# Kernel tuning notes

Hardware: AMD Instinct MI355X
Metric: run time of the kernel (lower is better)

Reference implementation:

```python
import jax, jax.numpy as jnp
import numpy as np

L = 3
NC = (L + 1) ** 2                                   # 16 spherical components l=0..3
SO3_SIZES = [(2 * l + 1) ** 2 for l in range(L + 1)]  # [1,9,25,49]
SO3_OFF = np.cumsum([0] + SO3_SIZES).tolist()         # [0,1,10,35,84]
D3 = SO3_OFF[-1]                                      # 84 = dim of SO(3) signal irreps
MUL_SIZES = [2 * l + 1 for l in range(L + 1)]         # [1,3,5,7]
MUL_OFF = np.cumsum([0] + MUL_SIZES).tolist()         # [0,1,4,9,16]
LIDX = jnp.array(sum([[l] * (2 * l + 1) for l in range(L + 1)], []))  # comp -> l map (16,)
B, NPG = 32, 256
N = B * NPG
E = 32768
F = 16
MAXR = 3.5
NG = 4096


def real_sh(v):
    # component-normalized real spherical harmonics l=0..3 for unit vectors v (...,3)
    x, y, z = v[..., 0], v[..., 1], v[..., 2]
    s3, s5, s15 = 3.0 ** 0.5, 5.0 ** 0.5, 15.0 ** 0.5
    c = [jnp.ones_like(x),
         s3 * y, s3 * z, s3 * x,
         s15 * x * y, s15 * y * z, 0.5 * s5 * (3 * z * z - 1.0), s15 * x * z, 0.5 * s15 * (x * x - y * y),
         (35.0 / 8.0) ** 0.5 * y * (3 * x * x - y * y),
         105.0 ** 0.5 * x * y * z,
         (21.0 / 8.0) ** 0.5 * y * (5 * z * z - 1.0),
         0.5 * 7.0 ** 0.5 * (5 * z ** 3 - 3 * z),
         (21.0 / 8.0) ** 0.5 * x * (5 * z * z - 1.0),
         0.5 * 105.0 ** 0.5 * (x * x - y * y) * z,
         (35.0 / 8.0) ** 0.5 * x * (x * x - 3 * y * y)]
    return jnp.stack(c, axis=-1)


def gate(h):
    # equivariant gate: relu on l=0 scalars, sigmoid(scalar)-gated l>0 components
    s = h[..., 0:1]
    return jnp.concatenate([jax.nn.relu(s), h[..., 1:] * jax.nn.sigmoid(s)], axis=-1)


def setup_inputs() -> dict:
    key = jax.random.key(0)
    ks = jax.random.split(key, 16)
    rn = lambda k, s, sc=1.0: jax.random.normal(k, s, dtype=jnp.float32) * sc
    return {
        'node_feat': rn(ks[0], (N, F)),
        'pos': rn(ks[1], (N, 3), 1.5),
        'orientation': jax.random.uniform(ks[2], (B, 2), dtype=jnp.float32) * jnp.pi,
        'rad1_W1': rn(ks[3], (1, 64)),
        'rad1_b': jnp.zeros((64,), jnp.float32),
        'rad1_W2': rn(ks[4], (64, 2048), 0.1),
        'rad2_W1': rn(ks[5], (1, 64)),
        'rad2_b': jnp.zeros((64,), jnp.float32),
        'rad2_W2': rn(ks[6], (64, 2176), 0.1),
        'Wlin': rn(ks[7], (2 * F, F, NC)),
        'psi1': rn(ks[8], (16, 64, D3)),
        'psi2': rn(ks[9], (64, 128, D3)),
        'psi3': rn(ks[10], (128, 256, D3)),
        'G_to': rn(ks[11], (D3, NG)),
        'G_from': rn(ks[12], (NG, D3)),
        'Ws2': rn(ks[13], (256, 1, NC)),
        'edge_src': jax.random.randint(ks[14], (E,), 0, N, dtype=jnp.int32),
        'edge_dst': jax.random.randint(ks[15], (E,), 0, N, dtype=jnp.int32),
        'batch': jnp.repeat(jnp.arange(B, dtype=jnp.int32), NPG),
    }


def reference(node_feat, pos, orientation, rad1_W1, rad1_b, rad1_W2, rad2_W1, rad2_b,
              rad2_W2, Wlin, psi1, psi2, psi3, G_to, G_from, Ws2,
              edge_src, edge_dst, batch):
    # ---- encoder: radius-graph equivariant message passing (gather / TP / scatter) ----
    ev = pos[edge_dst] - pos[edge_src]
    d = jnp.linalg.norm(ev, axis=-1) + 1e-9
    Y = real_sh(ev / d[:, None])                              # (E,16) edge SH
    u = d / MAXR
    cut = jnp.where(u < 1.0, 0.5 * (jnp.cos(jnp.pi * u) + 1.0), 0.0)

    def radial(W1, b, W2):
        hh = jax.nn.relu(u[:, None] * W1 + b)                 # (E,64)
        return (hh @ W2) * cut[:, None]

    deg = (E / N) ** 0.5
    # layer 1: scalar-in x SH tensor product with per-edge radial weights
    w1 = radial(rad1_W1, rad1_b, rad1_W2).reshape(E, F, F, 2, L + 1)
    t1 = jnp.einsum('ef,efgpl->egpl', node_feat[edge_src], w1) / (F ** 0.5)
    msg1 = t1[:, :, :, LIDX] * Y[:, None, None, :]            # (E,16,2,16)
    h1 = jax.ops.segment_sum(msg1, edge_dst, num_segments=N) / deg
    h1 = gate(h1)
    # layer 2: scalar x SH path + l_in (x) 0e self path
    w2 = radial(rad2_W1, rad2_b, rad2_W2)
    w2sh = w2[:, :2048].reshape(E, F, F, 2, L + 1)
    w2self = w2[:, 2048:].reshape(E, F, 2, L + 1)
    t2 = jnp.einsum('ef,efgpl->egpl', h1[:, :, 0, 0][edge_src], w2sh) / (F ** 0.5)
    msg2 = t2[:, :, :, LIDX] * Y[:, None, None, :] + h1[edge_src] * w2self[:, :, :, LIDX]
    h2 = jax.ops.segment_sum(msg2, edge_dst, num_segments=N) / deg
    h2 = gate(h2)
    # mean-pool readout per graph -> (B, 512)
    cnt = jax.ops.segment_sum(jnp.ones((N,), h2.dtype), batch, num_segments=B)
    enc = jax.ops.segment_sum(h2.reshape(N, -1), batch, num_segments=B) / cnt[:, None]

    # ---- o3.Linear enc_out -> so3_irreps latent z (B, F, 84) ----
    e = enc.reshape(B, 2 * F, NC)
    zs = []
    for l in range(L + 1):
        c0, c1 = MUL_OFF[l], MUL_OFF[l + 1]
        zl = jnp.einsum('bmc,mgj->bgjc', e[:, :, c0:c1], Wlin[:, :, c0:c1]) / (2 * F) ** 0.5
        zs.append(zl.reshape(B, F, -1))
    z = jnp.concatenate(zs, axis=-1)

    # ---- decoder: SO(3) equivariant convs + grid activations ----
    def so3_conv(x, psi):
        fi, fo = psi.shape[0], psi.shape[1]
        outs = []
        for l in range(L + 1):
            o0, o1 = SO3_OFF[l], SO3_OFF[l + 1]
            m = 2 * l + 1
            xl = x[:, :, o0:o1].reshape(B, fi, m, m)
            pl = psi[:, :, o0:o1].reshape(fi, fo, m, m)
            ol = jnp.einsum('bfic,fgij->bgjc', xl, pl) / (fi * m) ** 0.5
            outs.append(ol.reshape(B, fo, m * m))
        return jnp.concatenate(outs, axis=-1)

    def so3_act(x):
        g = jax.nn.relu(jnp.einsum('bfd,dg->bfg', x, G_to) / D3 ** 0.5)
        return jnp.einsum('bfg,gd->bfd', g, G_from) / NG ** 0.5

    x = so3_act(so3_conv(z, psi1))
    x = so3_act(so3_conv(x, psi2))
    x = so3_act(so3_conv(x, psi3))

    # ---- SO3 -> S2 convolution -> (B, out_dim, 16) ----
    outs = []
    for l in range(L + 1):
        o0, o1 = SO3_OFF[l], SO3_OFF[l + 1]
        m = 2 * l + 1
        xl = x[:, :, o0:o1].reshape(B, 256, m, m)
        Wl = Ws2[:, :, MUL_OFF[l]:MUL_OFF[l + 1]]
        outs.append(jnp.einsum('bfic,fgi->bgc', xl, Wl) / (256 * m) ** 0.5)
    s2 = jnp.concatenate(outs, axis=-1)

    # ---- aspect/roll -> cartesian line-of-sight -> SH response (bmm) ----
    a, r = orientation[..., 0], orientation[..., 1]
    cart = jnp.stack([-jnp.sin(a) * jnp.cos(r), -jnp.sin(a) * jnp.sin(r), -jnp.cos(a)], axis=-1)
    shp = real_sh(cart)                                       # (B,16)
    return jnp.einsum('bgc,bc->bg', s2, shp)[:, 0]            # (B,)
```

## Files before the change

kernel.cpp:

```cpp
#include <hip/hip_runtime.h>
#include <math.h>

#define DEV static __device__ __forceinline__

constexpr int NN = 8192;
constexpr int NE = 32768;
constexpr int NB = 32;

using short8 = __attribute__((ext_vector_type(8))) short;
using f32x4  = __attribute__((ext_vector_type(4))) float;

DEV ushort f2bf(float f) {
  unsigned u = __float_as_uint(f);
  unsigned r = (u + 0x7FFFu + ((u >> 16) & 1u)) >> 16;
  return (ushort)r;
}
DEV float bf2f(ushort h) { return __uint_as_float(((unsigned)h) << 16); }

DEV void split8(const float* p, short8& hi, short8& lo) {
#pragma unroll
  for (int j = 0; j < 8; ++j) {
    const ushort h = f2bf(p[j]);
    hi[j] = (short)h;
    const float r = p[j] - bf2f(h);
    lo[j] = (short)(__float_as_uint(r) >> 16);
  }
}

DEV int lidx_of(int c) { return (c == 0) ? 0 : (c < 4) ? 1 : (c < 9) ? 2 : 3; }

DEV void real_sh_f(float x, float y, float z, float* Y) {
  const float s3  = 1.7320508075688772f;
  const float s5  = 2.23606797749979f;
  const float s15 = 3.872983346207417f;
  Y[0] = 1.f;
  Y[1] = s3 * y;  Y[2] = s3 * z;  Y[3] = s3 * x;
  Y[4] = s15 * x * y;
  Y[5] = s15 * y * z;
  Y[6] = 0.5f * s5 * (3.f * z * z - 1.f);
  Y[7] = s15 * x * z;
  Y[8] = 0.5f * s15 * (x * x - y * y);
  Y[9]  = 2.091650066335189f * y * (3.f * x * x - y * y);
  Y[10] = 10.246950765959598f * x * y * z;
  Y[11] = 1.6201851746019651f * y * (5.f * z * z - 1.f);
  Y[12] = 1.3228756555322954f * (5.f * z * z * z - 3.f * z);
  Y[13] = 1.6201851746019651f * x * (5.f * z * z - 1.f);
  Y[14] = 5.123475382979799f * (x * x - y * y) * z;
  Y[15] = 2.091650066335189f * x * (x * x - 3.f * y * y);
}

__global__ __launch_bounds__(256) void k_edge_prep(
    const float* __restrict__ pos, const int* __restrict__ esrc,
    const int* __restrict__ edst, float* __restrict__ u_, float* __restrict__ cut_,
    float* __restrict__ Y_, int* __restrict__ cnt) {
  const int e = blockIdx.x * 256 + threadIdx.x;
  if (e >= NE) return;
  const int s = esrc[e], t = edst[e];
  const float ex = pos[t * 3 + 0] - pos[s * 3 + 0];
  const float ey = pos[t * 3 + 1] - pos[s * 3 + 1];
  const float ez = pos[t * 3 + 2] - pos[s * 3 + 2];
  const float d = sqrtf(ex * ex + ey * ey + ez * ez) + 1e-9f;
  const float inv = 1.f / d;
  float Y[16];
  real_sh_f(ex * inv, ey * inv, ez * inv, Y);
#pragma unroll
  for (int c = 0; c < 16; ++c) Y_[(size_t)e * 16 + c] = Y[c];
  const float u = d / 3.5f;
  u_[e] = u;
  cut_[e] = (u < 1.f) ? 0.5f * (cosf(3.14159265358979323846f * u) + 1.f) : 0.f;
  atomicAdd(&cnt[t], 1);
}

__global__ __launch_bounds__(256) void k_scan(const int* __restrict__ cnt,
                                              int* __restrict__ offs,
                                              int* __restrict__ cursor) {
  __shared__ int part[256];
  const int t = threadIdx.x;
  int s = 0;
  for (int i = 0; i < 32; ++i) s += cnt[t * 32 + i];
  part[t] = s;
  __syncthreads();
  if (t == 0) {
    int run = 0;
    for (int i = 0; i < 256; ++i) { int v = part[i]; part[i] = run; run += v; }
    offs[NN] = run;
  }
  __syncthreads();
  int run = part[t];
  for (int i = 0; i < 32; ++i) {
    const int idx = t * 32 + i;
    offs[idx] = run;
    cursor[idx] = run;
    run += cnt[idx];
  }
}

__global__ __launch_bounds__(256) void k_fill(const int* __restrict__ edst,
                                              int* __restrict__ cursor,
                                              int* __restrict__ elist) {
  const int e = blockIdx.x * 256 + threadIdx.x;
  if (e < NE) {
    const int p = atomicAdd(&cursor[edst[e]], 1);
    elist[p] = e;
  }
}

template <bool IS2>
__global__ __launch_bounds__(256) void k_prep_w2t(const float* __restrict__ W2,
                                                  ushort* __restrict__ Th,
                                                  ushort* __restrict__ Tl) {
  const int idx = blockIdx.x * 256 + threadIdx.x;
  if (idx >= 128 * 1024) return;
  const int o = idx >> 10, kf = idx & 1023;
  const float v = IS2 ? W2[(size_t)(kf >> 4) * 2176 + (kf & 15) * 128 + o]
                      : W2[(size_t)kf * 128 + o];
  const ushort h = f2bf(v);
  Th[idx] = h;
  Tl[idx] = (ushort)(__float_as_uint(v - bf2f(h)) >> 16);
}

__global__ __launch_bounds__(256) void k_prep_selfw(const float* __restrict__ W2,
                                                    ushort* __restrict__ Sh,
                                                    ushort* __restrict__ Sl) {
  const int idx = blockIdx.x * 256 + threadIdx.x;
  if (idx >= 128 * 64) return;
  const int o = idx >> 6, k = idx & 63;
  const float v = W2[(size_t)k * 2176 + 2048 + o];
  const ushort h = f2bf(v);
  Sh[idx] = h;
  Sl[idx] = (ushort)(__float_as_uint(v - bf2f(h)) >> 16);
}

#define MSG_STEP(HS, BH, BL)                                                     \
  do {                                                                           \
    short8 ah_[2], al_[2];                                                       \
    _Pragma("unroll") for (int mt = 0; mt < 2; ++mt) {                           \
      float p_[8];                                                               \
      _Pragma("unroll") for (int j = 0; j < 8; ++j) p_[j] = HS[mt] * nf8[mt][j]; \
      split8(p_, ah_[mt], al_[mt]);                                              \
    }                                                                            \
    _Pragma("unroll") for (int n = 0; n < 2; ++n) {                              \
      _Pragma("unroll") for (int mt = 0; mt < 2; ++mt) {                         \
        acc[mt][n] = __builtin_amdgcn_mfma_f32_16x16x32_bf16(ah_[mt], BH[n], acc[mt][n], 0, 0, 0); \
        acc[mt][n] = __builtin_amdgcn_mfma_f32_16x16x32_bf16(al_[mt], BH[n], acc[mt][n], 0, 0, 0); \
        acc[mt][n] = __builtin_amdgcn_mfma_f32_16x16x32_bf16(ah_[mt], BL[n], acc[mt][n], 0, 0, 0); \
      }                                                                          \
    }                                                                            \
  } while (0)

template <bool IS2>
__global__ __launch_bounds__(256) void k_msg_mfma(
    const float* __restrict__ u_, const float* __restrict__ cut_,
    const float* __restrict__ W1, const float* __restrict__ bvec,
    const ushort* __restrict__ W2Th, const ushort* __restrict__ W2Tl,
    const ushort* __restrict__ SWh, const ushort* __restrict__ SWl,
    const float* __restrict__ feat16, const int* __restrict__ esrc,
    float* __restrict__ t_, float* __restrict__ self_) {
  __shared__ float hhL[32 * 65];
  __shared__ float nfL[32 * 17];
  __shared__ float uL[32], cL[32];
  __shared__ int sL[32];
  const int tid = threadIdx.x;
  const int e0 = blockIdx.x * 32;
  if (tid < 32) {
    uL[tid] = u_[e0 + tid];
    cL[tid] = cut_[e0 + tid];
    sL[tid] = esrc[e0 + tid];
  }
  __syncthreads();
  for (int i = tid; i < 32 * 64; i += 256) {
    const int e = i >> 6, k = i & 63;
    hhL[e * 65 + k] = fmaxf(fmaf(uL[e], W1[k], bvec[k]), 0.f) * cL[e];
  }
  for (int i = tid; i < 32 * 16; i += 256) {
    const int e = i >> 4, f = i & 15;
    nfL[e * 17 + f] = feat16[(size_t)sL[e] * 16 + f];
  }
  __syncthreads();

  const int lane = tid & 63, wv = tid >> 6;
  const int lr = lane & 15, lg = lane >> 4;
  const int n0 = wv * 2;

  if (IS2) {
    f32x4 sacc[2][2];
#pragma unroll
    for (int mt = 0; mt < 2; ++mt)
#pragma unroll
      for (int n = 0; n < 2; ++n) {
        f32x4 zz = {0.f, 0.f, 0.f, 0.f};
        sacc[mt][n] = zz;
      }
#pragma unroll
    for (int ks2 = 0; ks2 < 2; ++ks2) {
      short8 ash[2], asl[2];
#pragma unroll
      for (int mt = 0; mt < 2; ++mt) {
        float p[8];
        const float* hp = &hhL[(mt * 16 + lr) * 65 + ks2 * 32 + lg * 8];
#pragma unroll
        for (int j = 0; j < 8; ++j) p[j] = hp[j];
        split8(p, ash[mt], asl[mt]);
      }
#pragma unroll
      for (int n = 0; n < 2; ++n) {
        const short8 bh = *(const short8*)&SWh[((n0 + n) * 16 + lr) * 64 + ks2 * 32 + lg * 8];
        const short8 bl = *(const short8*)&SWl[((n0 + n) * 16 + lr) * 64 + ks2 * 32 + lg * 8];
#pragma unroll
        for (int mt = 0; mt < 2; ++mt) {
          sacc[mt][n] = __builtin_amdgcn_mfma_f32_16x16x32_bf16(ash[mt], bh, sacc[mt][n], 0, 0, 0);
          sacc[mt][n] = __builtin_amdgcn_mfma_f32_16x16x32_bf16(asl[mt], bh, sacc[mt][n], 0, 0, 0);
          sacc[mt][n] = __builtin_amdgcn_mfma_f32_16x16x32_bf16(ash[mt], bl, sacc[mt][n], 0, 0, 0);
        }
      }
    }
#pragma unroll
    for (int mt = 0; mt < 2; ++mt)
#pragma unroll
      for (int n = 0; n < 2; ++n)
#pragma unroll
        for (int i = 0; i < 4; ++i)
          self_[(size_t)(e0 + mt * 16 + lg * 4 + i) * 128 + (n0 + n) * 16 + lr] =
              sacc[mt][n][i] * 0.5f;
  }

  float nf8[2][8];
#pragma unroll
  for (int mt = 0; mt < 2; ++mt)
#pragma unroll
    for (int j = 0; j < 8; ++j)
      nf8[mt][j] = nfL[(mt * 16 + lr) * 17 + (lg & 1) * 8 + j];

  f32x4 acc[2][2];
#pragma unroll
  for (int mt = 0; mt < 2; ++mt)
#pragma unroll
    for (int n = 0; n < 2; ++n) {
      f32x4 zz = {0.f, 0.f, 0.f, 0.f};
      acc[mt][n] = zz;
    }

  const ushort* bh_base[2] = {
    &W2Th[(size_t)((n0 + 0) * 16 + lr) * 1024 + lg * 8],
    &W2Th[(size_t)((n0 + 1) * 16 + lr) * 1024 + lg * 8]};
  const ushort* bl_base[2] = {
    &W2Tl[(size_t)((n0 + 0) * 16 + lr) * 1024 + lg * 8],
    &W2Tl[(size_t)((n0 + 1) * 16 + lr) * 1024 + lg * 8]};
  const float* hs_base[2] = {&hhL[(0 * 16 + lr) * 65 + (lg >> 1)],
                             &hhL[(1 * 16 + lr) * 65 + (lg >> 1)]};

  short8 bhA[2], blA[2], bhB[2], blB[2];
  float hsA[2], hsB[2];
#pragma unroll
  for (int n = 0; n < 2; ++n) {
    bhA[n] = *(const short8*)(bh_base[n]);
    blA[n] = *(const short8*)(bl_base[n]);
  }
  hsA[0] = hs_base[0][0];
  hsA[1] = hs_base[1][0];

  for (int ks = 0; ks < 32; ks += 2) {
#pragma unroll
    for (int n = 0; n < 2; ++n) {
      bhB[n] = *(const short8*)(bh_base[n] + (ks + 1) * 32);
      blB[n] = *(const short8*)(bl_base[n] + (ks + 1) * 32);
    }
    hsB[0] = hs_base[0][2 * (ks + 1)];
    hsB[1] = hs_base[1][2 * (ks + 1)];
    MSG_STEP(hsA, bhA, blA);
    if (ks + 2 < 32) {
#pragma unroll
      for (int n = 0; n < 2; ++n) {
        bhA[n] = *(const short8*)(bh_base[n] + (ks + 2) * 32);
        blA[n] = *(const short8*)(bl_base[n] + (ks + 2) * 32);
      }
      hsA[0] = hs_base[0][2 * (ks + 2)];
      hsA[1] = hs_base[1][2 * (ks + 2)];
    }
    MSG_STEP(hsB, bhB, blB);
  }
#pragma unroll
  for (int mt = 0; mt < 2; ++mt)
#pragma unroll
    for (int n = 0; n < 2; ++n)
#pragma unroll
      for (int i = 0; i < 4; ++i)
        t_[(size_t)(e0 + mt * 16 + lg * 4 + i) * 128 + (n0 + n) * 16 + lr] =
            acc[mt][n][i] * 0.125f;
}

__global__ __launch_bounds__(256) void k_gather1(
    const float* __restrict__ t_, const float* __restrict__ Y_,
    const int* __restrict__ offs, const int* __restrict__ elist,
    float* __restrict__ h1, float* __restrict__ h1s) {
  __shared__ float tL[128], YL[16], sG[32];
  const int n = blockIdx.x, tid = threadIdx.x;
  const int beg = offs[n], end = offs[n + 1];
  const int cc = tid & 15;
  const int lx = lidx_of(cc);
  const int o0 = ((tid >> 4) << 2) + lx;
  const int o1 = o0 + 64;
  float a0 = 0.f, a1 = 0.f;
  for (int ei = beg; ei < end; ++ei) {
    const int e = elist[ei];
    __syncthreads();
    if (tid < 128) tL[tid] = t_[(size_t)e * 128 + tid];
    else if (tid < 144) YL[tid - 128] = Y_[(size_t)e * 16 + tid - 128];
    __syncthreads();
    const float yv = YL[cc];
    a0 = fmaf(tL[o0], yv, a0);
    a1 = fmaf(tL[o1], yv, a1);
  }
  if (cc == 0) { sG[tid >> 4] = a0; sG[(tid >> 4) + 16] = a1; }
  __syncthreads();
  const float s0 = sG[tid >> 4], s1 = sG[(tid >> 4) + 16];
  const float r0 = (cc == 0) ? fmaxf(a0, 0.f) : a0 * (1.f / (1.f + expf(-s0)));
  const float r1 = (cc == 0) ? fmaxf(a1, 0.f) : a1 * (1.f / (1.f + expf(-s1)));
  h1[(size_t)n * 512 + tid] = r0;
  h1[(size_t)n * 512 + tid + 256] = r1;
  if ((tid & 31) == 0) {
    h1s[n * 16 + (tid >> 5)] = r0;
    h1s[n * 16 + (tid >> 5) + 8] = r1;
  }
}

__global__ __launch_bounds__(256) void k_gather2(
    const float* __restrict__ t_, const float* __restrict__ self_,
    const float* __restrict__ Y_, const float* __restrict__ h1,
    const int* __restrict__ offs, const int* __restrict__ elist,
    const int* __restrict__ esrc, float* __restrict__ h2) {
  __shared__ float tL[128], wL[128], YL[16], sG[32];
  const int n = blockIdx.x, tid = threadIdx.x;
  const int beg = offs[n], end = offs[n + 1];
  const int cc = tid & 15;
  const int lx = lidx_of(cc);
  const int o0 = ((tid >> 4) << 2) + lx;
  const int o1 = o0 + 64;
  float a0 = 0.f, a1 = 0.f;
  for (int ei = beg; ei < end; ++ei) {
    const int e = elist[ei];
    __syncthreads();
    if (tid < 128) tL[tid] = t_[(size_t)e * 128 + tid];
    else wL[tid - 128] = self_[(size_t)e * 128 + tid - 128];
    if (tid < 16) YL[tid] = Y_[(size_t)e * 16 + tid];
    __syncthreads();
    const int src = esrc[e];
    const float* hr = &h1[(size_t)src * 512];
    const float yv = YL[cc];
    a0 += tL[o0] * yv + hr[tid] * wL[o0];
    a1 += tL[o1] * yv + hr[tid + 256] * wL[o1];
  }
  if (cc == 0) { sG[tid >> 4] = a0; sG[(tid >> 4) + 16] = a1; }
  __syncthreads();
  const float s0 = sG[tid >> 4], s1 = sG[(tid >> 4) + 16];
  const float r0 = (cc == 0) ? fmaxf(a0, 0.f) : a0 * (1.f / (1.f + expf(-s0)));
  const float r1 = (cc == 0) ? fmaxf(a1, 0.f) : a1 * (1.f / (1.f + expf(-s1)));
  h2[(size_t)n * 512 + tid] = r0;
  h2[(size_t)n * 512 + tid + 256] = r1;
}

__global__ __launch_bounds__(256) void k_pool(const float* __restrict__ h2,
                                              float* __restrict__ enc) {
  const int b = blockIdx.x, tid = threadIdx.x;
  float a0 = 0.f, a1 = 0.f;
  for (int i = 0; i < 256; ++i) {
    const float* row = &h2[(size_t)(b * 256 + i) * 512];
    a0 += row[tid];
    a1 += row[tid + 256];
  }
  enc[b * 512 + tid] = a0 * (1.f / 256.f);
  enc[b * 512 + tid + 256] = a1 * (1.f / 256.f);
}

__global__ __launch_bounds__(256) void k_zproj(const float* __restrict__ enc,
                                               const float* __restrict__ Wlin,
                                               float* __restrict__ z) {
  __shared__ float eL[512];
  const int b = blockIdx.x, tid = threadIdx.x;
  eL[tid] = enc[b * 512 + tid];
  eL[tid + 256] = enc[b * 512 + tid + 256];
  __syncthreads();
  for (int idx = tid; idx < 16 * 84; idx += 256) {
    const int g = idx / 84, d3 = idx % 84;
    int o0, m0, mo;
    if (d3 < 1)       { o0 = 0;  m0 = 1; mo = 0; }
    else if (d3 < 10) { o0 = 1;  m0 = 3; mo = 1; }
    else if (d3 < 35) { o0 = 10; m0 = 5; mo = 4; }
    else              { o0 = 35; m0 = 7; mo = 9; }
    const int rem = d3 - o0;
    const int jj = rem / m0;
    const int cc2 = rem - jj * m0;
    float a = 0.f;
    for (int mu = 0; mu < 32; ++mu)
      a = fmaf(eL[mu * 16 + mo + cc2], Wlin[(mu * 16 + g) * 16 + mo + jj], a);
    z[(size_t)(b * 16 + g) * 84 + d3] = a * 0.17677669529663687f;
  }
}

template <int FI>
__global__ __launch_bounds__(256) void k_prep_xg(const float* __restrict__ x,
                                                 ushort* __restrict__ Xh,
                                                 ushort* __restrict__ Xl) {
  constexpr int KP0 = (FI + 31) & ~31, KP1 = (3 * FI + 31) & ~31;
  constexpr int KP2 = (5 * FI + 31) & ~31, KP3 = (7 * FI + 31) & ~31;
  constexpr int XO1 = 32 * KP0, XO2 = XO1 + 96 * KP1, XO3 = XO2 + 160 * KP2;
  constexpr int TOT = XO3 + 224 * KP3;
  const int idx = blockIdx.x * 256 + threadIdx.x;
  if (idx >= TOT) return;
  int m, o0, base, KP;
  if (idx < XO1)      { m = 1; o0 = 0;  base = 0;   KP = KP0; }
  else if (idx < XO2) { m = 3; o0 = 1;  base = XO1; KP = KP1; }
  else if (idx < XO3) { m = 5; o0 = 10; base = XO2; KP = KP2; }
  else                { m = 7; o0 = 35; base = XO3; KP = KP3; }
  const int rel = idx - base;
  const int r = rel / KP, k = rel % KP;
  ushort h = 0, lo = 0;
  if (k < FI * m) {
    const int f = k / m, i = k % m, b = r / m, c = r % m;
    const float v = x[((size_t)b * FI + f) * 84 + o0 + i * m + c];
    h = f2bf(v);
    lo = (ushort)(__float_as_uint(v - bf2f(h)) >> 16);
  }
  Xh[idx] = h;
  Xl[idx] = lo;
}

template <int FI, int FO>
__global__ __launch_bounds__(256) void k_prep_psig(const float* __restrict__ psi,
                                                   ushort* __restrict__ Ph,
                                                   ushort* __restrict__ Pl) {
  constexpr int KP0 = (FI + 31) & ~31, KP1 = (3 * FI + 31) & ~31;
  constexpr int KP2 = (5 * FI + 31) & ~31, KP3 = (7 * FI + 31) & ~31;
  constexpr int PO1 = FO * KP0, PO2 = PO1 + 3 * FO * KP1, PO3 = PO2 + 5 * FO * KP2;
  constexpr int TOT = PO3 + 7 * FO * KP3;
  const int idx = blockIdx.x * 256 + threadIdx.x;
  if (idx >= TOT) return;
  int m, o0, base, KP;
  if (idx < PO1)      { m = 1; o0 = 0;  base = 0;   KP = KP0; }
  else if (idx < PO2) { m = 3; o0 = 1;  base = PO1; KP = KP1; }
  else if (idx < PO3) { m = 5; o0 = 10; base = PO2; KP = KP2; }
  else                { m = 7; o0 = 35; base = PO3; KP = KP3; }
  const int rel = idx - base;
  const int n = rel / KP, k = rel % KP;
  ushort h = 0, lo = 0;
  if (k < FI * m) {
    const int f = k / m, i = k % m, g = n / m, j = n % m;
    const float v = psi[((size_t)f * FO + g) * 84 + o0 + i * m + j];
    h = f2bf(v);
    lo = (ushort)(__float_as_uint(v - bf2f(h)) >> 16);
  }
  Ph[idx] = h;
  Pl[idx] = lo;
}

template <int FI, int FO>
__global__ __launch_bounds__(256) void k_conv_gemm(
    const ushort* __restrict__ Xh, const ushort* __restrict__ Xl,
    const ushort* __restrict__ Ph, const ushort* __restrict__ Pl,
    float* __restrict__ out) {
  constexpr int KP0 = (FI + 31) & ~31, KP1 = (3 * FI + 31) & ~31;
  constexpr int KP2 = (5 * FI + 31) & ~31, KP3 = (7 * FI + 31) & ~31;
  constexpr int XO1 = 32 * KP0, XO2 = XO1 + 96 * KP1, XO3 = XO2 + 160 * KP2;
  constexpr int PO1 = FO * KP0, PO2 = PO1 + 3 * FO * KP1, PO3 = PO2 + 5 * FO * KP2;
  constexpr int NT0 = 1 * (FO / 32), NT1 = 3 * (3 * FO / 32);
  constexpr int NT2 = 5 * (5 * FO / 32), NT3 = 7 * (7 * FO / 32);
  constexpr int TB1 = NT0, TB2 = TB1 + NT1, TB3 = TB2 + NT2, TOT = TB3 + NT3;

  const int wt = blockIdx.x * 4 + (threadIdx.x >> 6);
  if (wt >= TOT) return;
  int m, o0, Mt, KP, Xo, Po, loc;
  if (wt < TB1)      { m = 1; o0 = 0;  Mt = 1; KP = KP0; Xo = 0;   Po = 0;   loc = wt; }
  else if (wt < TB2) { m = 3; o0 = 1;  Mt = 3; KP = KP1; Xo = XO1; Po = PO1; loc = wt - TB1; }
  else if (wt < TB3) { m = 5; o0 = 10; Mt = 5; KP = KP2; Xo = XO2; Po = PO2; loc = wt - TB2; }
  else               { m = 7; o0 = 35; Mt = 7; KP = KP3; Xo = XO3; Po = PO3; loc = wt - TB3; }
  const int mt0 = (loc % Mt) * 32;
  const int nt0 = (loc / Mt) * 32;
  const int lane = threadIdx.x & 63, lr = lane & 15, lg = lane >> 4;

  f32x4 acc[2][2];
#pragma unroll
  for (int mt = 0; mt < 2; ++mt)
#pragma unroll
    for (int nt = 0; nt < 2; ++nt) {
      f32x4 zz = {0.f, 0.f, 0.f, 0.f};
      acc[mt][nt] = zz;
    }

  const int nks = KP >> 5;
  for (int ks = 0; ks < nks; ++ks) {
    short8 ah[2], al[2], bh[2], bl[2];
#pragma unroll
    for (int t = 0; t < 2; ++t) {
      const size_t xa = (size_t)Xo + (size_t)(mt0 + t * 16 + lr) * KP + ks * 32 + lg * 8;
      ah[t] = *(const short8*)&Xh[xa];
      al[t] = *(const short8*)&Xl[xa];
      const size_t pa = (size_t)Po + (size_t)(nt0 + t * 16 + lr) * KP + ks * 32 + lg * 8;
      bh[t] = *(const short8*)&Ph[pa];
      bl[t] = *(const short8*)&Pl[pa];
    }
#pragma unroll
    for (int nt = 0; nt < 2; ++nt)
#pragma unroll
      for (int mt = 0; mt < 2; ++mt) {
        acc[mt][nt] = __builtin_amdgcn_mfma_f32_16x16x32_bf16(ah[mt], bh[nt], acc[mt][nt], 0, 0, 0);
        acc[mt][nt] = __builtin_amdgcn_mfma_f32_16x16x32_bf16(al[mt], bh[nt], acc[mt][nt], 0, 0, 0);
        acc[mt][nt] = __builtin_amdgcn_mfma_f32_16x16x32_bf16(ah[mt], bl[nt], acc[mt][nt], 0, 0, 0);
      }
  }

  const float scale = 1.f / sqrtf((float)(FI * m));
#pragma unroll
  for (int mt = 0; mt < 2; ++mt)
#pragma unroll
    for (int nt = 0; nt < 2; ++nt)
#pragma unroll
      for (int i = 0; i < 4; ++i) {
        const int R = mt0 + mt * 16 + lg * 4 + i;
        const int C2 = nt0 + nt * 16 + lr;
        const int b = R / m, c = R - b * m;
        const int g = C2 / m, j = C2 - g * m;
        out[((size_t)b * FO + g) * 84 + o0 + j * m + c] = acc[mt][nt][i] * scale;
      }
}

__global__ __launch_bounds__(256) void k_prep_gt(const float* __restrict__ Gt,
                                                 ushort* __restrict__ GtT) {
  const int idx = blockIdx.x * 256 + threadIdx.x;
  if (idx >= 4096 * 96) return;
  const int g = idx / 96, k = idx % 96;
  GtT[idx] = (k < 84) ? f2bf(Gt[(size_t)k * 4096 + g]) : (ushort)0;
}
__global__ __launch_bounds__(256) void k_prep_gf(const float* __restrict__ Gf,
                                                 ushort* __restrict__ GfT) {
  const int idx = blockIdx.x * 256 + threadIdx.x;
  if (idx >= 96 * 4096) return;
  const int d = idx / 4096, g = idx % 4096;
  GfT[idx] = (d < 84) ? f2bf(Gf[(size_t)g * 84 + d]) : (ushort)0;
}
__global__ __launch_bounds__(256) void k_cvtx(const float* __restrict__ x,
                                              ushort* __restrict__ Xb, int total) {
  const int idx = blockIdx.x * 256 + threadIdx.x;
  if (idx >= total) return;
  const int r = idx / 96, k = idx % 96;
  Xb[idx] = (k < 84) ? f2bf(x[(size_t)r * 84 + k]) : (ushort)0;
}

template <int GS>
__global__ __launch_bounds__(256) void k_act_mfma(
    const ushort* __restrict__ Xb, const ushort* __restrict__ GtT,
    const ushort* __restrict__ GfT, float* __restrict__ part, int NR) {
  constexpr int CPB = 64 / GS;
  __shared__ __align__(16) ushort ldsGt[64 * 104];
  __shared__ __align__(16) ushort ldsH[128 * 72];
  __shared__ __align__(16) ushort ldsGf[96 * 72];
  const int tid = threadIdx.x;
  const int gs = blockIdx.x;
  const int row0 = blockIdx.y * 128;
  const int lane = tid & 63, wv = tid >> 6;
  const int lr = lane & 15, lg = lane >> 4;
  const int m0 = wv * 32;

  short8 a1[2][3];
#pragma unroll
  for (int mt = 0; mt < 2; ++mt)
#pragma unroll
    for (int ks = 0; ks < 3; ++ks)
      a1[mt][ks] = *(const short8*)&Xb[(size_t)(row0 + m0 + mt * 16 + lr) * 96 +
                                       ks * 32 + lg * 8];

  f32x4 acc2[6][2];
#pragma unroll
  for (int m2 = 0; m2 < 6; ++m2)
#pragma unroll
    for (int n2 = 0; n2 < 2; ++n2) {
      f32x4 zz = {0.f, 0.f, 0.f, 0.f};
      acc2[m2][n2] = zz;
    }

  for (int ch = gs * CPB; ch < (gs + 1) * CPB; ++ch) {
    const int g0 = ch * 64;
    __syncthreads();
    for (int i = tid; i < 768; i += 256) {
      const int row = i / 12, c = i % 12;
      *(uint4*)&ldsGt[row * 104 + c * 8] =
          *(const uint4*)&GtT[(size_t)(g0 + row) * 96 + c * 8];
    }
    for (int i = tid; i < 768; i += 256) {
      const int row = i / 8, c = i % 8;
      *(uint4*)&ldsGf[row * 72 + c * 8] =
          *(const uint4*)&GfT[(size_t)row * 4096 + g0 + c * 8];
    }
    __syncthreads();
#pragma unroll
    for (int n = 0; n < 4; ++n) {
      short8 b[3];
#pragma unroll
      for (int ks = 0; ks < 3; ++ks)
        b[ks] = *(const short8*)&ldsGt[(n * 16 + lr) * 104 + ks * 32 + lg * 8];
#pragma unroll
      for (int mt = 0; mt < 2; ++mt) {
        f32x4 c1 = {0.f, 0.f, 0.f, 0.f};
#pragma unroll
        for (int ks = 0; ks < 3; ++ks)
          c1 = __builtin_amdgcn_mfma_f32_16x16x32_bf16(a1[mt][ks], b[ks], c1, 0, 0, 0);
        ushort* hp = &ldsH[(m0 + mt * 16 + lg * 4) * 72 + n * 16 + lr];
#pragma unroll
        for (int i = 0; i < 4; ++i) hp[i * 72] = f2bf(fmaxf(c1[i], 0.f));
      }
    }
#pragma unroll
    for (int k2 = 0; k2 < 2; ++k2) {
      short8 bh[2];
#pragma unroll
      for (int n2 = 0; n2 < 2; ++n2)
        bh[n2] = *(const short8*)&ldsH[(m0 + n2 * 16 + lr) * 72 + k2 * 32 + lg * 8];
#pragma unroll
      for (int m2 = 0; m2 < 6; ++m2) {
        const short8 a2 = *(const short8*)&ldsGf[(m2 * 16 + lr) * 72 + k2 * 32 + lg * 8];
        acc2[m2][0] = __builtin_amdgcn_mfma_f32_16x16x32_bf16(a2, bh[0], acc2[m2][0], 0, 0, 0);
        acc2[m2][1] = __builtin_amdgcn_mfma_f32_16x16x32_bf16(a2, bh[1], acc2[m2][1], 0, 0, 0);
      }
    }
  }
#pragma unroll
  for (int m2 = 0; m2 < 6; ++m2)
#pragma unroll
    for (int n2 = 0; n2 < 2; ++n2)
#pragma unroll
      for (int i = 0; i < 4; ++i) {
        const int d = m2 * 16 + lg * 4 + i;
        if (d < 84) {
          const int r = row0 + m0 + n2 * 16 + lr;
          part[((size_t)gs * NR + r) * 84 + d] = acc2[m2][n2][i];
        }
      }
}

template <int GS>
__global__ __launch_bounds__(256) void k_act_reduce(const float* __restrict__ part,
                                                    float* __restrict__ out, int total) {
  const int i = blockIdx.x * 256 + threadIdx.x;
  if (i < total) {
    float s = part[i];
#pragma unroll
    for (int g = 1; g < GS; ++g) s += part[(size_t)g * total + i];
    out[i] = s * (1.f / (9.16515138991168f * 64.f));
  }
}

__global__ __launch_bounds__(256) void k_final(const float* __restrict__ x,
                                               const float* __restrict__ Ws2,
                                               const float* __restrict__ orient,
                                               float* __restrict__ outp) {
  __shared__ float red[256][16];
  const int b = blockIdx.x, tid = threadIdx.x;
  const float* xr = &x[(size_t)(b * 256 + tid) * 84];
  const float* wr = &Ws2[tid * 16];
  float acc[16];
#pragma unroll
  for (int c = 0; c < 16; ++c) acc[c] = 0.f;
  acc[0] = fmaf(xr[0], wr[0], acc[0]);
#pragma unroll
  for (int i = 0; i < 3; ++i) {
    const float w = wr[1 + i];
#pragma unroll
    for (int c = 0; c < 3; ++c) acc[1 + c] = fmaf(xr[1 + i * 3 + c], w, acc[1 + c]);
  }
#pragma unroll
  for (int i = 0; i < 5; ++i) {
    const float w = wr[4 + i];
#pragma unroll
    for (int c = 0; c < 5; ++c) acc[4 + c] = fmaf(xr[10 + i * 5 + c], w, acc[4 + c]);
  }
#pragma unroll
  for (int i = 0; i < 7; ++i) {
    const float w = wr[9 + i];
#pragma unroll
    for (int c = 0; c < 7; ++c) acc[9 + c] = fmaf(xr[35 + i * 7 + c], w, acc[9 + c]);
  }
#pragma unroll
  for (int c = 0; c < 16; ++c) red[tid][c] = acc[c];
  __syncthreads();
  for (int off = 128; off > 0; off >>= 1) {
    if (tid < off)
#pragma unroll
      for (int c = 0; c < 16; ++c) red[tid][c] += red[tid + off][c];
    __syncthreads();
  }
  if (tid == 0) {
    const float aa = orient[b * 2 + 0], rr = orient[b * 2 + 1];
    float Y[16];
    real_sh_f(-sinf(aa) * cosf(rr), -sinf(aa) * sinf(rr), -cosf(aa), Y);
    const float sc1 = 1.f / 16.f;
    const float sc3 = 1.f / (16.f * 1.7320508075688772f);
    const float sc5 = 1.f / (16.f * 2.23606797749979f);
    const float sc7 = 1.f / (16.f * 2.6457513110645907f);
    float o = red[0][0] * sc1 * Y[0];
#pragma unroll
    for (int c = 1; c < 4; ++c) o += red[0][c] * sc3 * Y[c];
#pragma unroll
    for (int c = 4; c < 9; ++c) o += red[0][c] * sc5 * Y[c];
#pragma unroll
    for (int c = 9; c < 16; ++c) o += red[0][c] * sc7 * Y[c];
    outp[b] = o;
  }
}

extern "C" void kernel_launch(void* const* d_in, const int* in_sizes, int n_in,
                              void* d_out, int out_size, void* d_ws, size_t ws_size,
                              hipStream_t stream) {
  const float* node_feat = (const float*)d_in[0];
  const float* pos       = (const float*)d_in[1];
  const float* orient    = (const float*)d_in[2];
  const float* rad1_W1   = (const float*)d_in[3];
  const float* rad1_b    = (const float*)d_in[4];
  const float* rad1_W2   = (const float*)d_in[5];
  const float* rad2_W1   = (const float*)d_in[6];
  const float* rad2_b    = (const float*)d_in[7];
  const float* rad2_W2   = (const float*)d_in[8];
  const float* Wlin      = (const float*)d_in[9];
  const float* psi1      = (const float*)d_in[10];
  const float* psi2      = (const float*)d_in[11];
  const float* psi3      = (const float*)d_in[12];
  const float* G_to      = (const float*)d_in[13];
  const float* G_from    = (const float*)d_in[14];
  const float* Ws2       = (const float*)d_in[15];
  const int*   esrc      = (const int*)d_in[16];
  const int*   edst      = (const int*)d_in[17];

  float* w = (float*)d_ws;
  size_t off = 0;
  float* u_    = w + off; off += NE;
  float* cut_  = w + off; off += NE;
  float* Y_    = w + off; off += (size_t)NE * 16;
  float* t_    = w + off; off += (size_t)NE * 128;
  float* self_ = w + off; off += (size_t)NE * 128;
  float* h1    = w + off; off += (size_t)NN * 512;
  float* h1s   = w + off; off += (size_t)NN * 16;
  float* h2    = w + off; off += (size_t)NN * 512;
  float* enc   = w + off; off += (size_t)NB * 512;
  float* z     = w + off; off += (size_t)NB * 16 * 84;
  float* xb1   = w + off; off += (size_t)NB * 256 * 84;
  float* xb2   = w + off; off += (size_t)NB * 256 * 84;
  int* cnt    = (int*)(w + off); off += NN;
  int* offs   = (int*)(w + off); off += NN + 1;
  int* cursor = (int*)(w + off); off += NN;
  int* elist  = (int*)(w + off); off += NE;
  ushort* W2Th = (ushort*)(w + off); off += 65536;
  ushort* W2Tl = (ushort*)(w + off); off += 65536;
  ushort* SWh  = (ushort*)(w + off); off += 4096;
  ushort* SWl  = (ushort*)(w + off); off += 4096;

  float* part = t_;
  ushort* GtT = (ushort*)h1;
  ushort* GfT = GtT + 4096 * 96;
  ushort* Xb  = GfT + 96 * 4096;
  ushort* Xph = (ushort*)Y_;
  ushort* Xpl = Xph + 344064;
  ushort* Pph = (ushort*)h2;
  ushort* Ppl = Pph + 2752512;

  hipMemsetAsync(cnt, 0, NN * sizeof(int), stream);
  k_edge_prep<<<NE / 256, 256, 0, stream>>>(pos, esrc, edst, u_, cut_, Y_, cnt);
  k_scan<<<1, 256, 0, stream>>>(cnt, offs, cursor);
  k_fill<<<NE / 256, 256, 0, stream>>>(edst, cursor, elist);

  k_prep_w2t<false><<<512, 256, 0, stream>>>(rad1_W2, W2Th, W2Tl);
  k_msg_mfma<false><<<NE / 32, 256, 0, stream>>>(u_, cut_, rad1_W1, rad1_b, W2Th, W2Tl,
                                                 nullptr, nullptr, node_feat, esrc,
                                                 t_, nullptr);
  k_gather1<<<NN, 256, 0, stream>>>(t_, Y_, offs, elist, h1, h1s);

  k_prep_w2t<true><<<512, 256, 0, stream>>>(rad2_W2, W2Th, W2Tl);
  k_prep_selfw<<<32, 256, 0, stream>>>(rad2_W2, SWh, SWl);
  k_msg_mfma<true><<<NE / 32, 256, 0, stream>>>(u_, cut_, rad2_W1, rad2_b, W2Th, W2Tl,
                                                SWh, SWl, h1s, esrc, t_, self_);
  k_gather2<<<NN, 256, 0, stream>>>(t_, self_, Y_, h1, offs, elist, esrc, h2);
  k_pool<<<NB, 256, 0, stream>>>(h2, enc);
  k_zproj<<<NB, 256, 0, stream>>>(enc, Wlin, z);

  k_prep_gt<<<(4096 * 96 + 255) / 256, 256, 0, stream>>>(G_to, GtT);
  k_prep_gf<<<(96 * 4096 + 255) / 256, 256, 0, stream>>>(G_from, GfT);

  k_prep_psig<16, 64><<<(102400 + 255) / 256, 256, 0, stream>>>(psi1, Pph, Ppl);
  k_prep_xg<16><<<(51200 + 255) / 256, 256, 0, stream>>>(z, Xph, Xpl);
  k_conv_gemm<16, 64><<<42, 256, 0, stream>>>(Xph, Xpl, Pph, Ppl, xb1);
  k_cvtx<<<(2048 * 96 + 255) / 256, 256, 0, stream>>>(xb1, Xb, 2048 * 96);
  k_act_mfma<32><<<dim3(32, 16), 256, 0, stream>>>(Xb, GtT, GfT, part, 2048);
  k_act_reduce<32><<<(2048 * 84 + 255) / 256, 256, 0, stream>>>(part, xb2, 2048 * 84);

  k_prep_psig<64, 128><<<(688128 + 255) / 256, 256, 0, stream>>>(psi2, Pph, Ppl);
  k_prep_xg<64><<<(172032 + 255) / 256, 256, 0, stream>>>(xb2, Xph, Xpl);
  k_conv_gemm<64, 128><<<84, 256, 0, stream>>>(Xph, Xpl, Pph, Ppl, xb1);
  k_cvtx<<<(4096 * 96 + 255) / 256, 256, 0, stream>>>(xb1, Xb, 4096 * 96);
  k_act_mfma<16><<<dim3(16, 32), 256, 0, stream>>>(Xb, GtT, GfT, part, 4096);
  k_act_reduce<16><<<(4096 * 84 + 255) / 256, 256, 0, stream>>>(part, xb2, 4096 * 84);

  k_prep_psig<128, 256><<<(2752512 + 255) / 256, 256, 0, stream>>>(psi3, Pph, Ppl);
  k_prep_xg<128><<<(344064 + 255) / 256, 256, 0, stream>>>(xb2, Xph, Xpl);
  k_conv_gemm<128, 256><<<168, 256, 0, stream>>>(Xph, Xpl, Pph, Ppl, xb1);
  k_cvtx<<<(8192 * 96 + 255) / 256, 256, 0, stream>>>(xb1, Xb, 8192 * 96);
  k_act_mfma<8><<<dim3(8, 64), 256, 0, stream>>>(Xb, GtT, GfT, part, 8192);
  k_act_reduce<8><<<(8192 * 84 + 255) / 256, 256, 0, stream>>>(part, xb2, 8192 * 84);

  k_final<<<NB, 256, 0, stream>>>(xb2, Ws2, orient, (float*)d_out);
}
```

Measured before the change: 429.0 us.

## Switch message GEMM split to fp16 and double edges per block

The edge-message MFMA kernels now process 64 edges per block instead of 32, so each wave reuses every loaded W2 B-fragment across four M-tiles rather than two. This halves global weight traffic per edge. The hi/lo split precision moves from bf16 to fp16, using f16 MFMA and fp16-converted weight tables, which gives more mantissa bits per pass. The trade-offs are more accumulator registers per wave with lower occupancy, and fp16 range risk for the low residual terms.

After: 383.2 us. -10.7%, faster.

```diff
diff --git a/kernel.cpp b/kernel.cpp
--- a/kernel.cpp
+++ b/kernel.cpp
@@ -8,6 +8,7 @@
 constexpr int NB = 32;
 
 using short8 = __attribute__((ext_vector_type(8))) short;
+using half8  = __attribute__((ext_vector_type(8))) _Float16;
 using f32x4  = __attribute__((ext_vector_type(4))) float;
 
 DEV ushort f2bf(float f) {
@@ -17,13 +18,12 @@
 }
 DEV float bf2f(ushort h) { return __uint_as_float(((unsigned)h) << 16); }
 
-DEV void split8(const float* p, short8& hi, short8& lo) {
+DEV void split8h(const float* p, half8& hi, half8& lo) {
 #pragma unroll
   for (int j = 0; j < 8; ++j) {
-    const ushort h = f2bf(p[j]);
-    hi[j] = (short)h;
-    const float r = p[j] - bf2f(h);
-    lo[j] = (short)(__float_as_uint(r) >> 16);
+    const _Float16 h = (_Float16)p[j];
+    hi[j] = h;
+    lo[j] = (_Float16)(p[j] - (float)h);
   }
 }
 
@@ -114,9 +114,9 @@
   const int o = idx >> 10, kf = idx & 1023;
   const float v = IS2 ? W2[(size_t)(kf >> 4) * 2176 + (kf & 15) * 128 + o]
                       : W2[(size_t)kf * 128 + o];
-  const ushort h = f2bf(v);
-  Th[idx] = h;
-  Tl[idx] = (ushort)(__float_as_uint(v - bf2f(h)) >> 16);
+  const _Float16 h = (_Float16)v;
+  ((_Float16*)Th)[idx] = h;
+  ((_Float16*)Tl)[idx] = (_Float16)(v - (float)h);
 }
 
 __global__ __launch_bounds__(256) void k_prep_selfw(const float* __restrict__ W2,
@@ -126,24 +126,24 @@
   if (idx >= 128 * 64) return;
   const int o = idx >> 6, k = idx & 63;
   const float v = W2[(size_t)k * 2176 + 2048 + o];
-  const ushort h = f2bf(v);
-  Sh[idx] = h;
-  Sl[idx] = (ushort)(__float_as_uint(v - bf2f(h)) >> 16);
+  const _Float16 h = (_Float16)v;
+  ((_Float16*)Sh)[idx] = h;
+  ((_Float16*)Sl)[idx] = (_Float16)(v - (float)h);
 }
 
 #define MSG_STEP(HS, BH, BL)                                                     \
   do {                                                                           \
-    short8 ah_[2], al_[2];                                                       \
-    _Pragma("unroll") for (int mt = 0; mt < 2; ++mt) {                           \
+    half8 ah_[4], al_[4];                                                        \
+    _Pragma("unroll") for (int mt = 0; mt < 4; ++mt) {                           \
       float p_[8];                                                               \
       _Pragma("unroll") for (int j = 0; j < 8; ++j) p_[j] = HS[mt] * nf8[mt][j]; \
-      split8(p_, ah_[mt], al_[mt]);                                              \
+      split8h(p_, ah_[mt], al_[mt]);                                             \
     }                                                                            \
     _Pragma("unroll") for (int n = 0; n < 2; ++n) {                              \
-      _Pragma("unroll") for (int mt = 0; mt < 2; ++mt) {                         \
-        acc[mt][n] = __builtin_amdgcn_mfma_f32_16x16x32_bf16(ah_[mt], BH[n], acc[mt][n], 0, 0, 0); \
-        acc[mt][n] = __builtin_amdgcn_mfma_f32_16x16x32_bf16(al_[mt], BH[n], acc[mt][n], 0, 0, 0); \
-        acc[mt][n] = __builtin_amdgcn_mfma_f32_16x16x32_bf16(ah_[mt], BL[n], acc[mt][n], 0, 0, 0); \
+      _Pragma("unroll") for (int mt = 0; mt < 4; ++mt) {                         \
+        acc[mt][n] = __builtin_amdgcn_mfma_f32_16x16x32_f16(ah_[mt], BH[n], acc[mt][n], 0, 0, 0); \
+        acc[mt][n] = __builtin_amdgcn_mfma_f32_16x16x32_f16(al_[mt], BH[n], acc[mt][n], 0, 0, 0); \
+        acc[mt][n] = __builtin_amdgcn_mfma_f32_16x16x32_f16(ah_[mt], BL[n], acc[mt][n], 0, 0, 0); \
       }                                                                          \
     }                                                                            \
   } while (0)
@@ -156,23 +156,23 @@
     const ushort* __restrict__ SWh, const ushort* __restrict__ SWl,
     const float* __restrict__ feat16, const int* __restrict__ esrc,
     float* __restrict__ t_, float* __restrict__ self_) {
-  __shared__ float hhL[32 * 65];
-  __shared__ float nfL[32 * 17];
-  __shared__ float uL[32], cL[32];
-  __shared__ int sL[32];
+  __shared__ float hhL[64 * 65];
+  __shared__ float nfL[64 * 17];
+  __shared__ float uL[64], cL[64];
+  __shared__ int sL[64];
   const int tid = threadIdx.x;
-  const int e0 = blockIdx.x * 32;
-  if (tid < 32) {
+  const int e0 = blockIdx.x * 64;
+  if (tid < 64) {
     uL[tid] = u_[e0 + tid];
     cL[tid] = cut_[e0 + tid];
     sL[tid] = esrc[e0 + tid];
   }
   __syncthreads();
-  for (int i = tid; i < 32 * 64; i += 256) {
+  for (int i = tid; i < 64 * 64; i += 256) {
     const int e = i >> 6, k = i & 63;
     hhL[e * 65 + k] = fmaxf(fmaf(uL[e], W1[k], bvec[k]), 0.f) * cL[e];
   }
-  for (int i = tid; i < 32 * 16; i += 256) {
+  for (int i = tid; i < 64 * 16; i += 256) {
     const int e = i >> 4, f = i & 15;
     nfL[e * 17 + f] = feat16[(size_t)sL[e] * 16 + f];
   }
@@ -183,9 +183,9 @@
   const int n0 = wv * 2;
 
   if (IS2) {
-    f32x4 sacc[2][2];
-#pragma unroll
-    for (int mt = 0; mt < 2; ++mt)
+    f32x4 sacc[4][2];
+#pragma unroll
+    for (int mt = 0; mt < 4; ++mt)
 #pragma unroll
       for (int n = 0; n < 2; ++n) {
         f32x4 zz = {0.f, 0.f, 0.f, 0.f};
@@ -193,29 +193,29 @@
       }
 #pragma unroll
     for (int ks2 = 0; ks2 < 2; ++ks2) {
-      short8 ash[2], asl[2];
-#pragma unroll
-      for (int mt = 0; mt < 2; ++mt) {
+      half8 ash[4], asl[4];
+#pragma unroll
+      for (int mt = 0; mt < 4; ++mt) {
         float p[8];
         const float* hp = &hhL[(mt * 16 + lr) * 65 + ks2 * 32 + lg * 8];
 #pragma unroll
         for (int j = 0; j < 8; ++j) p[j] = hp[j];
-        split8(p, ash[mt], asl[mt]);
+        split8h(p, ash[mt], asl[mt]);
       }
 #pragma unroll
       for (int n = 0; n < 2; ++n) {
-        const short8 bh = *(const short8*)&SWh[((n0 + n) * 16 + lr) * 64 + ks2 * 32 + lg * 8];
-        const short8 bl = *(const short8*)&SWl[((n0 + n) * 16 + lr) * 64 + ks2 * 32 + lg * 8];
-#pragma unroll
-        for (int mt = 0; mt < 2; ++mt) {
-          sacc[mt][n] = __builtin_amdgcn_mfma_f32_16x16x32_bf16(ash[mt], bh, sacc[mt][n], 0, 0, 0);
-          sacc[mt][n] = __builtin_amdgcn_mfma_f32_16x16x32_bf16(asl[mt], bh, sacc[mt][n], 0, 0, 0);
-          sacc[mt][n] = __builtin_amdgcn_mfma_f32_16x16x32_bf16(ash[mt], bl, sacc[mt][n], 0, 0, 0);
+        const half8 bh = *(const half8*)&SWh[((n0 + n) * 16 + lr) * 64 + ks2 * 32 + lg * 8];
+        const half8 bl = *(const half8*)&SWl[((n0 + n) * 16 + lr) * 64 + ks2 * 32 + lg * 8];
+#pragma unroll
+        for (int mt = 0; mt < 4; ++mt) {
+          sacc[mt][n] = __builtin_amdgcn_mfma_f32_16x16x32_f16(ash[mt], bh, sacc[mt][n], 0, 0, 0);
+          sacc[mt][n] = __builtin_amdgcn_mfma_f32_16x16x32_f16(asl[mt], bh, sacc[mt][n], 0, 0, 0);
+          sacc[mt][n] = __builtin_amdgcn_mfma_f32_16x16x32_f16(ash[mt], bl, sacc[mt][n], 0, 0, 0);
         }
       }
     }
 #pragma unroll
-    for (int mt = 0; mt < 2; ++mt)
+    for (int mt = 0; mt < 4; ++mt)
 #pragma unroll
       for (int n = 0; n < 2; ++n)
 #pragma unroll
@@ -224,16 +224,16 @@
               sacc[mt][n][i] * 0.5f;
   }
 
-  float nf8[2][8];
-#pragma unroll
-  for (int mt = 0; mt < 2; ++mt)
+  float nf8[4][8];
+#pragma unroll
+  for (int mt = 0; mt < 4; ++mt)
 #pragma unroll
     for (int j = 0; j < 8; ++j)
       nf8[mt][j] = nfL[(mt * 16 + lr) * 17 + (lg & 1) * 8 + j];
 
-  f32x4 acc[2][2];
-#pragma unroll
-  for (int mt = 0; mt < 2; ++mt)
+  f32x4 acc[4][2];
+#pragma unroll
+  for (int mt = 0; mt < 4; ++mt)
 #pragma unroll
     for (int n = 0; n < 2; ++n) {
       f32x4 zz = {0.f, 0.f, 0.f, 0.f};
@@ -246,41 +246,43 @@
   const ushort* bl_base[2] = {
     &W2Tl[(size_t)((n0 + 0) * 16 + lr) * 1024 + lg * 8],
     &W2Tl[(size_t)((n0 + 1) * 16 + lr) * 1024 + lg * 8]};
-  const float* hs_base[2] = {&hhL[(0 * 16 + lr) * 65 + (lg >> 1)],
-                             &hhL[(1 * 16 + lr) * 65 + (lg >> 1)]};
-
-  short8 bhA[2], blA[2], bhB[2], blB[2];
-  float hsA[2], hsB[2];
+  const float* hs_base[4] = {&hhL[(0 * 16 + lr) * 65 + (lg >> 1)],
+                             &hhL[(1 * 16 + lr) * 65 + (lg >> 1)],
+                             &hhL[(2 * 16 + lr) * 65 + (lg >> 1)],
+                             &hhL[(3 * 16 + lr) * 65 + (lg >> 1)]};
+
+  half8 bhA[2], blA[2], bhB[2], blB[2];
+  float hsA[4], hsB[4];
 #pragma unroll
   for (int n = 0; n < 2; ++n) {
-    bhA[n] = *(const short8*)(bh_base[n]);
-    blA[n] = *(const short8*)(bl_base[n]);
-  }
-  hsA[0] = hs_base[0][0];
-  hsA[1] = hs_base[1][0];
+    bhA[n] = *(const half8*)(bh_base[n]);
+    blA[n] = *(const half8*)(bl_base[n]);
+  }
+#pragma unroll
+  for (int mt = 0; mt < 4; ++mt) hsA[mt] = hs_base[mt][0];
 
   for (int ks = 0; ks < 32; ks += 2) {
 #pragma unroll
     for (int n = 0; n < 2; ++n) {
-      bhB[n] = *(const short8*)(bh_base[n] + (ks + 1) * 32);
-      blB[n] = *(const short8*)(bl_base[n] + (ks + 1) * 32);
-    }
-    hsB[0] = hs_base[0][2 * (ks + 1)];
-    hsB[1] = hs_base[1][2 * (ks + 1)];
+      bhB[n] = *(const half8*)(bh_base[n] + (ks + 1) * 32);
+      blB[n] = *(const half8*)(bl_base[n] + (ks + 1) * 32);
+    }
+#pragma unroll
+    for (int mt = 0; mt < 4; ++mt) hsB[mt] = hs_base[mt][2 * (ks + 1)];
     MSG_STEP(hsA, bhA, blA);
     if (ks + 2 < 32) {
 #pragma unroll
       for (int n = 0; n < 2; ++n) {
-        bhA[n] = *(const short8*)(bh_base[n] + (ks + 2) * 32);
-        blA[n] = *(const short8*)(bl_base[n] + (ks + 2) * 32);
+        bhA[n] = *(const half8*)(bh_base[n] + (ks + 2) * 32);
+        blA[n] = *(const half8*)(bl_base[n] + (ks + 2) * 32);
       }
-      hsA[0] = hs_base[0][2 * (ks + 2)];
-      hsA[1] = hs_base[1][2 * (ks + 2)];
+#pragma unroll
+      for (int mt = 0; mt < 4; ++mt) hsA[mt] = hs_base[mt][2 * (ks + 2)];
     }
     MSG_STEP(hsB, bhB, blB);
   }
 #pragma unroll
-  for (int mt = 0; mt < 2; ++mt)
+  for (int mt = 0; mt < 4; ++mt)
 #pragma unroll
     for (int n = 0; n < 2; ++n)
 #pragma unroll
@@ -766,14 +768,14 @@
   k_fill<<<NE / 256, 256, 0, stream>>>(edst, cursor, elist);
 
   k_prep_w2t<false><<<512, 256, 0, stream>>>(rad1_W2, W2Th, W2Tl);
-  k_msg_mfma<false><<<NE / 32, 256, 0, stream>>>(u_, cut_, rad1_W1, rad1_b, W2Th, W2Tl,
+  k_msg_mfma<false><<<NE / 64, 256, 0, stream>>>(u_, cut_, rad1_W1, rad1_b, W2Th, W2Tl,
                                                  nullptr, nullptr, node_feat, esrc,
                                                  t_, nullptr);
   k_gather1<<<NN, 256, 0, stream>>>(t_, Y_, offs, elist, h1, h1s);
 
   k_prep_w2t<true><<<512, 256, 0, stream>>>(rad2_W2, W2Th, W2Tl);
   k_prep_selfw<<<32, 256, 0, stream>>>(rad2_W2, SWh, SWl);
-  k_msg_mfma<true><<<NE / 32, 256, 0, stream>>>(u_, cut_, rad2_W1, rad2_b, W2Th, W2Tl,
+  k_msg_mfma<true><<<NE / 64, 256, 0, stream>>>(u_, cut_, rad2_W1, rad2_b, W2Th, W2Tl,
                                                 SWh, SWl, h1s, esrc, t_, self_);
   k_gather2<<<NN, 256, 0, stream>>>(t_, self_, Y_, h1, offs, elist, esrc, h2);
   k_pool<<<NB, 256, 0, stream>>>(h2, enc);
```
